# Performance work log

Measured on AMD Instinct MI355X. Metric: run time of the kernel, lower is better.

## Reference

```python
import jax, jax.numpy as jnp
import numpy as np

N, E = 100000, 1600000
IN, H, Z, C = 64, 128, 64, 2


def _glorot(key, fan_in, fan_out):
    s = jnp.sqrt(2.0 / (fan_in + fan_out)).astype(jnp.float32)
    return jax.random.normal(key, (fan_in, fan_out), dtype=jnp.float32) * s


def setup_inputs() -> dict:
    key = jax.random.key(0)
    ks = jax.random.split(key, 16)
    dims = [(IN, H), (H, H), (H, Z), (H, H), (H, Z), (Z, H), (H, H), (H, IN * C)]
    names = ['in', 'mu0', 'mu', 'si0', 'si', 'z', 'd0', 'out']
    inp = {
        'x': jax.random.normal(ks[0], (N, IN), dtype=jnp.float32),
        'eps': jax.random.normal(ks[1], (N, Z), dtype=jnp.float32),
        'edge_index': jax.random.randint(ks[2], (2, E), 0, N, dtype=jnp.int64),
    }
    for i, (nm, (fi, fo)) in enumerate(zip(names, dims)):
        inp[f'w_{nm}'] = _glorot(ks[3 + i], fi, fo)
        inp[f'b_{nm}'] = jnp.zeros((fo,), dtype=jnp.float32)
    return inp


def _gcn(x, W, b, src, dst, dinv):
    # PyG GCNConv: symmetric normalization with self-loops.
    h = x @ W                                      # [N, d_out]
    norm = (dinv[src] * dinv[dst])[:, None]        # [E, 1]
    agg = jax.ops.segment_sum(h[src] * norm, dst, num_segments=N)
    agg = agg + h * (dinv * dinv)[:, None]         # self-loop term (norm = 1/deg)
    return agg + b


def reference(x, edge_index, eps,
              w_in, b_in, w_mu0, b_mu0, w_mu, b_mu,
              w_si0, b_si0, w_si, b_si,
              w_z, b_z, w_d0, b_d0, w_out, b_out):
    src, dst = edge_index[0], edge_index[1]
    deg = jax.ops.segment_sum(jnp.ones((E,), jnp.float32), dst, num_segments=N) + 1.0
    dinv = jax.lax.rsqrt(deg)
    # encode
    h = jax.nn.relu(_gcn(x, w_in, b_in, src, dst, dinv))
    mu = jax.nn.relu(_gcn(h, w_mu0, b_mu0, src, dst, dinv))
    mu = jax.nn.relu(_gcn(mu, w_mu, b_mu, src, dst, dinv))
    si = jax.nn.relu(_gcn(h, w_si0, b_si0, src, dst, dinv))
    si = jax.nn.sigmoid(_gcn(si, w_si, b_si, src, dst, dinv))
    # reparameterize
    z = mu + si * eps
    # decode (first decoder layer has no activation, per the original forward)
    r = _gcn(z, w_z, b_z, src, dst, dinv)
    r = jax.nn.relu(_gcn(r, w_d0, b_d0, src, dst, dinv))
    logits = _gcn(r, w_out, b_out, src, dst, dinv)   # [N, IN*C]
    logits = logits.reshape(-1, C)                   # [N*IN, C]
    return logits, mu, si
```

## Files before the change

### kernel.cpp

```cpp
#include <hip/hip_runtime.h>


typedef short bf16x8 __attribute__((ext_vector_type(8)));
typedef float f32x4 __attribute__((ext_vector_type(4)));

__device__ __forceinline__ ushort f2bf(float f) {
    uint x = __float_as_uint(f);
    uint r = x + 0x7FFFu + ((x >> 16) & 1u);
    return (ushort)(r >> 16);
}
__device__ __forceinline__ float bf2f(ushort h) {
    return __uint_as_float(((uint)h) << 16);
}

__global__ void count_deg_kernel(const int* __restrict__ dst, int* __restrict__ deg, int E) {
    int i = blockIdx.x * blockDim.x + threadIdx.x;
    if (i < E) atomicAdd(&deg[dst[i]], 1);
}

__global__ void dinv_kernel(const int* __restrict__ deg, float* __restrict__ dinv, int N) {
    int i = blockIdx.x * blockDim.x + threadIdx.x;
    if (i < N) dinv[i] = rsqrtf((float)(deg[i] + 1));
}

__global__ __launch_bounds__(1024) void scan_block_kernel(const int* __restrict__ deg,
                                                          int* __restrict__ row_start,
                                                          int* __restrict__ bsum, int n) {
    __shared__ int s[1024];
    int i = blockIdx.x * 1024 + threadIdx.x;
    int v = (i < n) ? deg[i] : 0;
    s[threadIdx.x] = v;
    __syncthreads();
    for (int off = 1; off < 1024; off <<= 1) {
        int t = (threadIdx.x >= off) ? s[threadIdx.x - off] : 0;
        __syncthreads();
        s[threadIdx.x] += t;
        __syncthreads();
    }
    if (i < n) row_start[i] = s[threadIdx.x] - v;
    if (threadIdx.x == 1023) bsum[blockIdx.x] = s[1023];
}

__global__ __launch_bounds__(1024) void scan_partials_kernel(int* __restrict__ bsum, int nb) {
    __shared__ int s[1024];
    int v = (threadIdx.x < nb) ? bsum[threadIdx.x] : 0;
    s[threadIdx.x] = v;
    __syncthreads();
    for (int off = 1; off < 1024; off <<= 1) {
        int t = (threadIdx.x >= off) ? s[threadIdx.x - off] : 0;
        __syncthreads();
        s[threadIdx.x] += t;
        __syncthreads();
    }
    if (threadIdx.x < nb) bsum[threadIdx.x] = s[threadIdx.x] - v;
}

__global__ __launch_bounds__(1024) void scan_add_kernel(int* __restrict__ row_start,
                                                        const int* __restrict__ bsum, int N, int E) {
    int i = blockIdx.x * 1024 + threadIdx.x;
    if (i < N) row_start[i] += bsum[blockIdx.x];
    if (i == 0) row_start[N] = E;
}

__global__ void place_kernel(const int* __restrict__ src, const int* __restrict__ dst,
                             const int* __restrict__ row_start, int* __restrict__ cnt,
                             int2* __restrict__ csr, const float* __restrict__ dinv, int E) {
    int i = blockIdx.x * blockDim.x + threadIdx.x;
    if (i < E) {
        int d = dst[i], s = src[i];
        int pos = row_start[d] + atomicAdd(&cnt[d], 1);
        csr[pos] = make_int2(s, __float_as_int(dinv[s] * dinv[d]));
    }
}

__global__ void rowsum_kernel(const int2* __restrict__ csr, const int* __restrict__ row_start,
                              const float* __restrict__ dinv, float* __restrict__ cvec, int N) {
    int j = blockIdx.x * blockDim.x + threadIdx.x;
    if (j >= N) return;
    float s = dinv[j] * dinv[j];
    int b = row_start[j], e = row_start[j + 1];
    for (int k = b; k < e; ++k) s += __int_as_float(csr[k].y);
    cvec[j] = s;
}

__global__ void wc_kernel(const float* __restrict__ w_z, const float* __restrict__ b_z,
                          const float* __restrict__ w_d0,
                          float* __restrict__ Wc, float* __restrict__ bzw) {
    int o = blockIdx.x * 256 + threadIdx.x;
    if (o >= 65 * 128) return;
    int i = o >> 7, j = o & 127;
    float s = 0.f;
    for (int k = 0; k < 128; ++k) {
        float a = (i < 64) ? w_z[i * 128 + k] : b_z[k];
        s = fmaf(a, w_d0[k * 128 + j], s);
    }
    if (i < 64) Wc[i * 128 + j] = s;
    else        bzw[j] = s;
}

__global__ void pack_kernel(const float* __restrict__ W, ushort* __restrict__ Wp, int KI, int KO) {
    int idx = blockIdx.x * 256 + threadIdx.x;
    if (idx >= KI * KO) return;
    int e = idx & 7, l = (idx >> 3) & 63, t = idx >> 9;
    int KB = KI / 32;
    int c = t / KB, kb = t % KB;
    int k = kb * 32 + (l >> 4) * 8 + e, col = c * 16 + (l & 15);
    Wp[idx] = f2bf(W[(size_t)k * KO + col]);
}

__global__ void cvt8_kernel(const float* __restrict__ in, ushort* __restrict__ out, int n8) {
    int i = blockIdx.x * 256 + threadIdx.x;
    if (i >= n8) return;
    float4 a = ((const float4*)in)[i * 2];
    float4 b = ((const float4*)in)[i * 2 + 1];
    bf16x8 o;
    o[0] = (short)f2bf(a.x); o[1] = (short)f2bf(a.y);
    o[2] = (short)f2bf(a.z); o[3] = (short)f2bf(a.w);
    o[4] = (short)f2bf(b.x); o[5] = (short)f2bf(b.y);
    o[6] = (short)f2bf(b.z); o[7] = (short)f2bf(b.w);
    ((bf16x8*)out)[i] = o;
}

template <int W, int EPI, int OUT>
__global__ __launch_bounds__(256) void bprop_kernel(const ushort* __restrict__ xb, void* __restrict__ outp,
                                                    const int* __restrict__ row_start,
                                                    const int2* __restrict__ csr,
                                                    const float* __restrict__ dinv,
                                                    const float* __restrict__ bias,
                                                    const float* __restrict__ mu,
                                                    const float* __restrict__ eps,
                                                    ushort* __restrict__ zout, int N) {
    constexpr int L = W / 8;
    constexpr int EPL = 64 / L;
    int wave = threadIdx.x >> 6, lane = threadIdx.x & 63;
    int node = blockIdx.x * 4 + wave;
    if (node >= N) return;
    int sub = lane / L, f8 = lane % L;
    int beg = row_start[node], end = row_start[node + 1];
    float d2 = dinv[node]; d2 = d2 * d2;

    float a0[8] = {}, a1[8] = {};
    for (int base = beg; base < end; base += 2 * EPL) {
        int e0 = base + sub, e1 = base + EPL + sub;
        int2 p0 = csr[e0 < end ? e0 : 0];
        int2 p1 = csr[e1 < end ? e1 : 0];
        float w0 = (e0 < end) ? __int_as_float(p0.y) : 0.f;
        float w1 = (e1 < end) ? __int_as_float(p1.y) : 0.f;
        bf16x8 v0 = *(const bf16x8*)(xb + (size_t)p0.x * W + f8 * 8);
        bf16x8 v1 = *(const bf16x8*)(xb + (size_t)p1.x * W + f8 * 8);
        #pragma unroll
        for (int i = 0; i < 8; ++i) a0[i] = fmaf(w0, bf2f((ushort)v0[i]), a0[i]);
        #pragma unroll
        for (int i = 0; i < 8; ++i) a1[i] = fmaf(w1, bf2f((ushort)v1[i]), a1[i]);
    }
    float acc[8];
    #pragma unroll
    for (int i = 0; i < 8; ++i) acc[i] = a0[i] + a1[i];
    #pragma unroll
    for (int m = L; m < 64; m <<= 1) {
        #pragma unroll
        for (int i = 0; i < 8; ++i) acc[i] += __shfl_xor(acc[i], m);
    }
    if (sub != 0) return;

    bf16x8 sv = *(const bf16x8*)(xb + (size_t)node * W + f8 * 8);
    #pragma unroll
    for (int i = 0; i < 8; ++i) acc[i] = fmaf(d2, bf2f((ushort)sv[i]), acc[i]);

    if constexpr (EPI >= 1) {
        float4 b0 = *(const float4*)&bias[f8 * 8];
        float4 b1 = *(const float4*)&bias[f8 * 8 + 4];
        float bv[8] = {b0.x, b0.y, b0.z, b0.w, b1.x, b1.y, b1.z, b1.w};
        if constexpr (EPI == 1) {
            #pragma unroll
            for (int i = 0; i < 8; ++i) acc[i] = fmaxf(acc[i] + bv[i], 0.f);
        } else {
            #pragma unroll
            for (int i = 0; i < 8; ++i) acc[i] = 1.f / (1.f + __expf(-(acc[i] + bv[i])));
        }
    }

    if constexpr (OUT == 0) {
        bf16x8 o;
        #pragma unroll
        for (int i = 0; i < 8; ++i) o[i] = (short)f2bf(acc[i]);
        ((bf16x8*)outp)[(size_t)node * L + f8] = o;
    } else {
        float* of = (float*)outp;
        *(float4*)&of[(size_t)node * W + f8 * 8]     = make_float4(acc[0], acc[1], acc[2], acc[3]);
        *(float4*)&of[(size_t)node * W + f8 * 8 + 4] = make_float4(acc[4], acc[5], acc[6], acc[7]);
    }
    if constexpr (EPI == 2) {
        float4 m0 = *(const float4*)&mu[(size_t)node * W + f8 * 8];
        float4 m1 = *(const float4*)&mu[(size_t)node * W + f8 * 8 + 4];
        float4 e0 = *(const float4*)&eps[(size_t)node * W + f8 * 8];
        float4 e1 = *(const float4*)&eps[(size_t)node * W + f8 * 8 + 4];
        float mv[8] = {m0.x, m0.y, m0.z, m0.w, m1.x, m1.y, m1.z, m1.w};
        float ev[8] = {e0.x, e0.y, e0.z, e0.w, e1.x, e1.y, e1.z, e1.w};
        bf16x8 z;
        #pragma unroll
        for (int i = 0; i < 8; ++i) z[i] = (short)f2bf(fmaf(acc[i], ev[i], mv[i]));
        ((bf16x8*)zout)[(size_t)node * L + f8] = z;
    }
}

template <int KI, int KO, int EPI, int OUT>
__global__ __launch_bounds__(256) void mgemm_kernel(const ushort* __restrict__ Xb,
                                                    const bf16x8* __restrict__ Wp,
                                                    const float* __restrict__ bias,
                                                    const float* __restrict__ bias2,
                                                    const float* __restrict__ cvec,
                                                    void* __restrict__ outp, int N) {
    constexpr int KB = KI / 32;
    constexpr int CT = KO / 16;
    constexpr size_t LSB = (OUT == 1) ? (size_t)64 * KO * 4 : (size_t)64 * KO * 2;
    __shared__ __align__(16) char LsRaw[LSB];

    int w = threadIdx.x >> 6, l = threadIdx.x & 63;
    int lr = l & 15, lk = l >> 4;
    int rowbase = blockIdx.x * 64;
    int r0 = rowbase + w * 16;

    int arow = r0 + lr; if (arow > N - 1) arow = N - 1;
    bf16x8 a[KB];
    const ushort* xp = Xb + (size_t)arow * KI + lk * 8;
    #pragma unroll
    for (int kb = 0; kb < KB; ++kb) a[kb] = *(const bf16x8*)(xp + kb * 32);

    float cv[4];
    if constexpr (EPI == 3) {
        #pragma unroll
        for (int r = 0; r < 4; ++r) {
            int rr = r0 + lk * 4 + r;
            cv[r] = cvec[rr < N ? rr : 0];
        }
    }

    #pragma unroll
    for (int c = 0; c < CT; ++c) {
        f32x4 acc = {0.f, 0.f, 0.f, 0.f};
        #pragma unroll
        for (int kb = 0; kb < KB; ++kb)
            acc = __builtin_amdgcn_mfma_f32_16x16x32_bf16(a[kb], Wp[((size_t)c * KB + kb) * 64 + l], acc, 0, 0, 0);
        int col = c * 16 + lr;
        float bv = 0.f, b2v = 0.f;
        if constexpr (EPI >= 1) bv = bias[col];
        if constexpr (EPI == 3) b2v = bias2[col];
        #pragma unroll
        for (int r = 0; r < 4; ++r) {
            float v = acc[r];
            if constexpr (EPI == 1) v += bv;
            if constexpr (EPI == 2) v = fmaxf(v + bv, 0.f);
            if constexpr (EPI == 3) v = fmaxf(v + cv[r] * bv + b2v, 0.f);
            int rl = w * 16 + lk * 4 + r;
            if constexpr (OUT == 0) ((ushort*)LsRaw)[(size_t)rl * KO + col] = f2bf(v);
            else                    ((float*)LsRaw)[(size_t)rl * KO + col] = v;
        }
    }
    __syncthreads();

    if constexpr (OUT == 0) {
        ushort* o = (ushort*)outp;
        constexpr int CH = 64 * KO / 8;
        for (int idx = threadIdx.x; idx < CH; idx += 256) {
            int row = idx / (KO / 8), c8 = idx % (KO / 8);
            if (rowbase + row < N)
                *(bf16x8*)(o + (size_t)(rowbase + row) * KO + c8 * 8) = ((const bf16x8*)LsRaw)[idx];
        }
    } else {
        float* o = (float*)outp;
        constexpr int CH = 64 * KO / 4;
        for (int idx = threadIdx.x; idx < CH; idx += 256) {
            int row = idx / (KO / 4), c4 = idx % (KO / 4);
            if (rowbase + row < N)
                *(float4*)(o + (size_t)(rowbase + row) * KO + c4 * 4) = ((const float4*)LsRaw)[idx];
        }
    }
}

extern "C" void kernel_launch(void* const* d_in, const int* in_sizes, int n_in,
                              void* d_out, int out_size, void* d_ws, size_t ws_size,
                              hipStream_t stream) {
    const float* x    = (const float*)d_in[0];
    const float* eps  = (const float*)d_in[1];
    const int*   ei   = (const int*)d_in[2];
    const float* w_in  = (const float*)d_in[3];  const float* b_in  = (const float*)d_in[4];
    const float* w_mu0 = (const float*)d_in[5];  const float* b_mu0 = (const float*)d_in[6];
    const float* w_mu  = (const float*)d_in[7];  const float* b_mu  = (const float*)d_in[8];
    const float* w_si0 = (const float*)d_in[9];  const float* b_si0 = (const float*)d_in[10];
    const float* w_si  = (const float*)d_in[11]; const float* b_si  = (const float*)d_in[12];
    const float* w_z   = (const float*)d_in[13]; const float* b_z   = (const float*)d_in[14];
    const float* w_d0  = (const float*)d_in[15]; const float* b_d0  = (const float*)d_in[16];
    const float* w_out = (const float*)d_in[17]; const float* b_out = (const float*)d_in[18];

    const int N = in_sizes[0] / 64;
    const int E = in_sizes[2] / 2;
    const int* srcI = ei;
    const int* dstI = ei + E;

    auto align = [](size_t v) { return (v + 255) & ~(size_t)255; };
    char* w = (char*)d_ws;
    size_t off = 0;
    int*    deg       = (int*)(w + off);    off = align(off + (size_t)N * 4);
    float*  cvec      = (float*)(w + off);  off = align(off + (size_t)N * 4);
    int*    row_start = (int*)(w + off);    off = align(off + (size_t)(N + 1) * 4);
    int*    bsum      = (int*)(w + off);    off = align(off + 1024 * 4);
    float*  dinv      = (float*)(w + off);  off = align(off + (size_t)N * 4);
    float*  Wc        = (float*)(w + off);  off = align(off + 64 * 128 * 4);
    float*  bzw       = (float*)(w + off);  off = align(off + 128 * 4);
    ushort* P_in      = (ushort*)(w + off); off = align(off + 64 * 128 * 2);
    ushort* P_mu0     = (ushort*)(w + off); off = align(off + 128 * 128 * 2);
    ushort* P_si0     = (ushort*)(w + off); off = align(off + 128 * 128 * 2);
    ushort* P_mu      = (ushort*)(w + off); off = align(off + 128 * 64 * 2);
    ushort* P_si      = (ushort*)(w + off); off = align(off + 128 * 64 * 2);
    ushort* P_wc      = (ushort*)(w + off); off = align(off + 64 * 128 * 2);
    ushort* P_out     = (ushort*)(w + off); off = align(off + 128 * 128 * 2);
    int2*   csr       = (int2*)(w + off);   off = align(off + (size_t)E * 8);
    ushort* xb        = (ushort*)(w + off); off = align(off + (size_t)N * 64 * 2);
    ushort* Ab        = (ushort*)(w + off); off = align(off + (size_t)N * 128 * 2);
    ushort* Ab0 = Ab;
    ushort* Ab1 = Ab + (size_t)N * 64;

    float* Cc = (float*)d_out;
    float* M  = Cc + (size_t)N * 128;
    float* S  = M + (size_t)N * 64;
    ushort* Cb_x = (ushort*)Cc;
    ushort* Cb_y = (ushort*)(Cc + (size_t)N * 64);
    ushort* Db_x = (ushort*)M;

    const int TB = 256;
    hipMemsetAsync(deg, 0, (size_t)N * 4, stream);
    count_deg_kernel<<<(E + TB - 1) / TB, TB, 0, stream>>>(dstI, deg, E);
    dinv_kernel<<<(N + TB - 1) / TB, TB, 0, stream>>>(deg, dinv, N);
    int nb = (N + 1023) / 1024;
    scan_block_kernel<<<nb, 1024, 0, stream>>>(deg, row_start, bsum, N);
    scan_partials_kernel<<<1, 1024, 0, stream>>>(bsum, nb);
    scan_add_kernel<<<nb, 1024, 0, stream>>>(row_start, bsum, N, E);
    hipMemsetAsync(deg, 0, (size_t)N * 4, stream);
    place_kernel<<<(E + TB - 1) / TB, TB, 0, stream>>>(srcI, dstI, row_start, deg, csr, dinv, E);
    rowsum_kernel<<<(N + TB - 1) / TB, TB, 0, stream>>>(csr, row_start, dinv, cvec, N);
    wc_kernel<<<(65 * 128 + 255) / 256, 256, 0, stream>>>(w_z, b_z, w_d0, Wc, bzw);

    pack_kernel<<<(64 * 128 + 255) / 256, 256, 0, stream>>>(w_in, P_in, 64, 128);
    pack_kernel<<<(128 * 128 + 255) / 256, 256, 0, stream>>>(w_mu0, P_mu0, 128, 128);
    pack_kernel<<<(128 * 128 + 255) / 256, 256, 0, stream>>>(w_si0, P_si0, 128, 128);
    pack_kernel<<<(128 * 64 + 255) / 256, 256, 0, stream>>>(w_mu, P_mu, 128, 64);
    pack_kernel<<<(128 * 64 + 255) / 256, 256, 0, stream>>>(w_si, P_si, 128, 64);
    pack_kernel<<<(64 * 128 + 255) / 256, 256, 0, stream>>>(Wc, P_wc, 64, 128);
    pack_kernel<<<(128 * 128 + 255) / 256, 256, 0, stream>>>(w_out, P_out, 128, 128);
    cvt8_kernel<<<((N * 8) + 255) / 256, 256, 0, stream>>>(x, xb, N * 8);

    int pgrid = (N + 3) / 4;
    int ggrid = (N + 63) / 64;

    bprop_kernel<64, 0, 0><<<pgrid, 256, 0, stream>>>(xb, Ab0, row_start, csr, dinv, nullptr, nullptr, nullptr, nullptr, N);
    mgemm_kernel<64, 128, 2, 0><<<ggrid, 256, 0, stream>>>(Ab0, (const bf16x8*)P_in, b_in, nullptr, nullptr, Cb_x, N);
    bprop_kernel<128, 0, 0><<<pgrid, 256, 0, stream>>>(Cb_x, Db_x, row_start, csr, dinv, nullptr, nullptr, nullptr, nullptr, N);
    mgemm_kernel<128, 128, 2, 0><<<ggrid, 256, 0, stream>>>(Db_x, (const bf16x8*)P_mu0, b_mu0, nullptr, nullptr, Ab, N);
    mgemm_kernel<128, 128, 2, 0><<<ggrid, 256, 0, stream>>>(Db_x, (const bf16x8*)P_si0, b_si0, nullptr, nullptr, Cb_x, N);
    mgemm_kernel<128, 64, 0, 0><<<ggrid, 256, 0, stream>>>(Ab, (const bf16x8*)P_mu, nullptr, nullptr, nullptr, Cb_y, N);
    bprop_kernel<64, 1, 1><<<pgrid, 256, 0, stream>>>(Cb_y, M, row_start, csr, dinv, b_mu, nullptr, nullptr, nullptr, N);
    mgemm_kernel<128, 64, 0, 0><<<ggrid, 256, 0, stream>>>(Cb_x, (const bf16x8*)P_si, nullptr, nullptr, nullptr, Ab0, N);
    bprop_kernel<64, 2, 1><<<pgrid, 256, 0, stream>>>(Ab0, S, row_start, csr, dinv, b_si, M, eps, Ab1, N);
    bprop_kernel<64, 0, 0><<<pgrid, 256, 0, stream>>>(Ab1, Cb_y, row_start, csr, dinv, nullptr, nullptr, nullptr, nullptr, N);
    bprop_kernel<64, 0, 0><<<pgrid, 256, 0, stream>>>(Cb_y, Ab0, row_start, csr, dinv, nullptr, nullptr, nullptr, nullptr, N);
    mgemm_kernel<64, 128, 3, 0><<<ggrid, 256, 0, stream>>>(Ab0, (const bf16x8*)P_wc, bzw, b_d0, cvec, Cb_x, N);
    bprop_kernel<128, 0, 0><<<pgrid, 256, 0, stream>>>(Cb_x, Ab, row_start, csr, dinv, nullptr, nullptr, nullptr, nullptr, N);
    mgemm_kernel<128, 128, 1, 1><<<ggrid, 256, 0, stream>>>(Ab, (const bf16x8*)P_out, b_out, nullptr, nullptr, Cc, N);
}
```

Baseline: 622.1 us.

## Fuse gather with MFMA GEMMs per layer and bin edges before CSR placement

Aggregation (gather over CSR) and the following bf16 MFMA GEMMs are fused into single kernels per layer that stage 64-row tiles in LDS. The mu and sigma encoder branches now share one gathered tile, and their two 64-wide outputs are packed into one 128-wide buffer so they are propagated together. This removes intermediate global round-trips and many launches. CSR construction gains a two-pass binned scatter meant to improve locality of the placement atomics, and the weight pack kernels are merged into one launch. The cost is that gather work runs serialized before the GEMM within a block, with lower occupancy from larger LDS use, and there are extra passes over the edges.

New measurement: 809.1 us. 1.3x slower.

```diff
diff --git a/kernel.cpp b/kernel.cpp
--- a/kernel.cpp
+++ b/kernel.cpp
@@ -13,9 +13,22 @@
     return __uint_as_float(((uint)h) << 16);
 }
 
-__global__ void count_deg_kernel(const int* __restrict__ dst, int* __restrict__ deg, int E) {
-    int i = blockIdx.x * blockDim.x + threadIdx.x;
-    if (i < E) atomicAdd(&deg[dst[i]], 1);
+__global__ __launch_bounds__(1024) void counts_kernel(const int* __restrict__ dst,
+        int* __restrict__ deg, int* __restrict__ bc0, int E, int NB, int shift) {
+    __shared__ int h[8192];
+    for (int j = threadIdx.x; j < NB; j += 1024) h[j] = 0;
+    __syncthreads();
+    int stride = gridDim.x * 1024;
+    for (int i = blockIdx.x * 1024 + threadIdx.x; i < E; i += stride) {
+        int d = dst[i];
+        atomicAdd(&deg[d], 1);
+        atomicAdd(&h[d >> shift], 1);
+    }
+    __syncthreads();
+    for (int j = threadIdx.x; j < NB; j += 1024) {
+        int v = h[j];
+        if (v) atomicAdd(&bc0[j], v);
+    }
 }
 
 __global__ void dinv_kernel(const int* __restrict__ deg, float* __restrict__ dinv, int N) {
@@ -23,12 +36,12 @@
     if (i < N) dinv[i] = rsqrtf((float)(deg[i] + 1));
 }
 
-__global__ __launch_bounds__(1024) void scan_block_kernel(const int* __restrict__ deg,
-                                                          int* __restrict__ row_start,
+__global__ __launch_bounds__(1024) void scan_block_kernel(const int* __restrict__ in,
+                                                          int* __restrict__ out,
                                                           int* __restrict__ bsum, int n) {
     __shared__ int s[1024];
     int i = blockIdx.x * 1024 + threadIdx.x;
-    int v = (i < n) ? deg[i] : 0;
+    int v = (i < n) ? in[i] : 0;
     s[threadIdx.x] = v;
     __syncthreads();
     for (int off = 1; off < 1024; off <<= 1) {
@@ -37,7 +50,7 @@
         s[threadIdx.x] += t;
         __syncthreads();
     }
-    if (i < n) row_start[i] = s[threadIdx.x] - v;
+    if (i < n) out[i] = s[threadIdx.x] - v;
     if (threadIdx.x == 1023) bsum[blockIdx.x] = s[1023];
 }
 
@@ -55,21 +68,33 @@
     if (threadIdx.x < nb) bsum[threadIdx.x] = s[threadIdx.x] - v;
 }
 
-__global__ __launch_bounds__(1024) void scan_add_kernel(int* __restrict__ row_start,
-                                                        const int* __restrict__ bsum, int N, int E) {
+__global__ __launch_bounds__(1024) void scan_add_kernel(int* __restrict__ arr,
+                                                        const int* __restrict__ bsum, int n, int total) {
     int i = blockIdx.x * 1024 + threadIdx.x;
-    if (i < N) row_start[i] += bsum[blockIdx.x];
-    if (i == 0) row_start[N] = E;
-}
-
-__global__ void place_kernel(const int* __restrict__ src, const int* __restrict__ dst,
-                             const int* __restrict__ row_start, int* __restrict__ cnt,
-                             int2* __restrict__ csr, const float* __restrict__ dinv, int E) {
+    if (i < n) arr[i] += bsum[blockIdx.x];
+    if (i == 0) arr[n] = total;
+}
+
+__global__ void scatter_kernel(const int* __restrict__ src, const int* __restrict__ dst,
+                               const int* __restrict__ bin_start, int* __restrict__ bc1,
+                               int2* __restrict__ ebuf, int E, int shift) {
     int i = blockIdx.x * blockDim.x + threadIdx.x;
     if (i < E) {
-        int d = dst[i], s = src[i];
-        int pos = row_start[d] + atomicAdd(&cnt[d], 1);
-        csr[pos] = make_int2(s, __float_as_int(dinv[s] * dinv[d]));
+        int d = dst[i];
+        int b = d >> shift;
+        int pos = bin_start[b] + atomicAdd(&bc1[b], 1);
+        ebuf[pos] = make_int2(src[i], d);
+    }
+}
+
+__global__ void place2_kernel(const int2* __restrict__ ebuf, const int* __restrict__ row_start,
+                              int* __restrict__ cnt, int2* __restrict__ csr,
+                              const float* __restrict__ dinv, int E) {
+    int i = blockIdx.x * blockDim.x + threadIdx.x;
+    if (i < E) {
+        int2 e = ebuf[i];
+        int pos = row_start[e.y] + atomicAdd(&cnt[e.y], 1);
+        csr[pos] = make_int2(e.x, __float_as_int(dinv[e.x] * dinv[e.y]));
     }
 }
 
@@ -83,9 +108,9 @@
     cvec[j] = s;
 }
 
-__global__ void wc_kernel(const float* __restrict__ w_z, const float* __restrict__ b_z,
-                          const float* __restrict__ w_d0,
-                          float* __restrict__ Wc, float* __restrict__ bzw) {
+__global__ void wcpack_kernel(const float* __restrict__ w_z, const float* __restrict__ b_z,
+                              const float* __restrict__ w_d0,
+                              ushort* __restrict__ P_wc, float* __restrict__ bzw) {
     int o = blockIdx.x * 256 + threadIdx.x;
     if (o >= 65 * 128) return;
     int i = o >> 7, j = o & 127;
@@ -94,18 +119,33 @@
         float a = (i < 64) ? w_z[i * 128 + k] : b_z[k];
         s = fmaf(a, w_d0[k * 128 + j], s);
     }
-    if (i < 64) Wc[i * 128 + j] = s;
-    else        bzw[j] = s;
-}
-
-__global__ void pack_kernel(const float* __restrict__ W, ushort* __restrict__ Wp, int KI, int KO) {
-    int idx = blockIdx.x * 256 + threadIdx.x;
+    if (i < 64) {
+        int c = j >> 4, kb = i >> 5, l = ((i >> 3) & 3) * 16 + (j & 15), e = i & 7;
+        P_wc[(size_t)((c * 2 + kb) * 64 + l) * 8 + e] = f2bf(s);
+    } else bzw[j] = s;
+}
+
+__device__ __forceinline__ void pack_one(const float* __restrict__ W, ushort* __restrict__ P,
+                                         int KI, int KO, int idx) {
     if (idx >= KI * KO) return;
     int e = idx & 7, l = (idx >> 3) & 63, t = idx >> 9;
     int KB = KI / 32;
     int c = t / KB, kb = t % KB;
-    int k = kb * 32 + (l >> 4) * 8 + e, col = c * 16 + (l & 15);
-    Wp[idx] = f2bf(W[(size_t)k * KO + col]);
+    int k = kb * 32 + ((l >> 4) << 3) + e, col = c * 16 + (l & 15);
+    P[idx] = f2bf(W[(size_t)k * KO + col]);
+}
+
+__global__ void megapack_kernel(const float* w_in, const float* w_mu0, const float* w_si0,
+                                const float* w_mu, const float* w_si, const float* w_out,
+                                ushort* P_in, ushort* P_mu0, ushort* P_si0,
+                                ushort* P_mu, ushort* P_si, ushort* P_out) {
+    int b = blockIdx.x, tid = threadIdx.x;
+    if (b < 32)       pack_one(w_in,  P_in,  64, 128,  (b - 0)   * 256 + tid);
+    else if (b < 96)  pack_one(w_mu0, P_mu0, 128, 128, (b - 32)  * 256 + tid);
+    else if (b < 160) pack_one(w_si0, P_si0, 128, 128, (b - 96)  * 256 + tid);
+    else if (b < 192) pack_one(w_mu,  P_mu,  128, 64,  (b - 160) * 256 + tid);
+    else if (b < 224) pack_one(w_si,  P_si,  128, 64,  (b - 192) * 256 + tid);
+    else              pack_one(w_out, P_out, 128, 128, (b - 224) * 256 + tid);
 }
 
 __global__ void cvt8_kernel(const float* __restrict__ in, ushort* __restrict__ out, int n8) {
@@ -121,24 +161,194 @@
     ((bf16x8*)out)[i] = o;
 }
 
-template <int W, int EPI, int OUT>
-__global__ __launch_bounds__(256) void bprop_kernel(const ushort* __restrict__ xb, void* __restrict__ outp,
-                                                    const int* __restrict__ row_start,
-                                                    const int2* __restrict__ csr,
-                                                    const float* __restrict__ dinv,
-                                                    const float* __restrict__ bias,
-                                                    const float* __restrict__ mu,
-                                                    const float* __restrict__ eps,
-                                                    ushort* __restrict__ zout, int N) {
-    constexpr int L = W / 8;
-    constexpr int EPL = 64 / L;
+
+template <int WI>
+__device__ __forceinline__ void gather_phase(char* Ls, const ushort* __restrict__ xb,
+        const int* __restrict__ row_start, const int2* __restrict__ csr,
+        const float* __restrict__ dinv, int rowbase, int N, int tid) {
+    constexpr int L = WI / 8, EPL = 64 / L;
+    constexpr int STR = WI * 2 + 16;
+    int w = tid >> 6, lane = tid & 63;
+    int sub = lane / L, f8 = lane % L;
+    #pragma unroll 1
+    for (int i = 0; i < 16; ++i) {
+        int lrow = w * 16 + i;
+        int node = rowbase + lrow;
+        float acc[8] = {0.f, 0.f, 0.f, 0.f, 0.f, 0.f, 0.f, 0.f};
+        if (node < N) {
+            int beg = row_start[node], end = row_start[node + 1];
+            float d2 = dinv[node]; d2 *= d2;
+            float a0[8] = {}, a1[8] = {};
+            for (int base = beg; base < end; base += 2 * EPL) {
+                int e0 = base + sub, e1 = base + EPL + sub;
+                int2 p0 = csr[e0 < end ? e0 : 0];
+                int2 p1 = csr[e1 < end ? e1 : 0];
+                float w0 = (e0 < end) ? __int_as_float(p0.y) : 0.f;
+                float w1 = (e1 < end) ? __int_as_float(p1.y) : 0.f;
+                bf16x8 v0 = *(const bf16x8*)(xb + (size_t)p0.x * WI + f8 * 8);
+                bf16x8 v1 = *(const bf16x8*)(xb + (size_t)p1.x * WI + f8 * 8);
+                #pragma unroll
+                for (int q = 0; q < 8; ++q) a0[q] = fmaf(w0, bf2f((ushort)v0[q]), a0[q]);
+                #pragma unroll
+                for (int q = 0; q < 8; ++q) a1[q] = fmaf(w1, bf2f((ushort)v1[q]), a1[q]);
+            }
+            #pragma unroll
+            for (int q = 0; q < 8; ++q) acc[q] = a0[q] + a1[q];
+            #pragma unroll
+            for (int m = L; m < 64; m <<= 1) {
+                #pragma unroll
+                for (int q = 0; q < 8; ++q) acc[q] += __shfl_xor(acc[q], m);
+            }
+            bf16x8 sv = *(const bf16x8*)(xb + (size_t)node * WI + f8 * 8);
+            #pragma unroll
+            for (int q = 0; q < 8; ++q) acc[q] = fmaf(d2, bf2f((ushort)sv[q]), acc[q]);
+        }
+        if (sub == 0) {
+            bf16x8 o;
+            #pragma unroll
+            for (int q = 0; q < 8; ++q) o[q] = (short)f2bf(acc[q]);
+            *(bf16x8*)(Ls + lrow * STR + f8 * 16) = o;
+        }
+    }
+}
+
+template <int KI, int KO>
+__device__ __forceinline__ void mfma_phase(const char* Ls, const bf16x8* __restrict__ Wp,
+                                           float (*acc)[4], int tid) {
+    constexpr int KB = KI / 32, CT = KO / 16, STR = KI * 2 + 16;
+    int w = tid >> 6, l = tid & 63;
+    int row = w * 16 + (l & 15);
+    int lk = l >> 4;
+    bf16x8 a[KB];
+    #pragma unroll
+    for (int kb = 0; kb < KB; ++kb)
+        a[kb] = *(const bf16x8*)(Ls + row * STR + kb * 64 + lk * 16);
+    #pragma unroll
+    for (int c = 0; c < CT; ++c) {
+        f32x4 v = {0.f, 0.f, 0.f, 0.f};
+        #pragma unroll
+        for (int kb = 0; kb < KB; ++kb)
+            v = __builtin_amdgcn_mfma_f32_16x16x32_bf16(a[kb], Wp[((size_t)c * KB + kb) * 64 + l], v, 0, 0, 0);
+        acc[c][0] = v[0]; acc[c][1] = v[1]; acc[c][2] = v[2]; acc[c][3] = v[3];
+    }
+}
+
+template <int DW>
+__device__ __forceinline__ void cstore_bf16(char* Ls, const float* v, int cbase, int tid) {
+    constexpr int STR = DW * 2 + 16;
+    int w = tid >> 6, l = tid & 63;
+    int col = cbase + (l & 15);
+    int row0 = w * 16 + (l >> 4) * 4;
+    #pragma unroll
+    for (int r = 0; r < 4; ++r)
+        *(ushort*)(Ls + (row0 + r) * STR + col * 2) = f2bf(v[r]);
+}
+
+template <int KO>
+__device__ __forceinline__ void flush_bf16(const char* Ls, ushort* __restrict__ out,
+                                           int rowbase, int N, int tid) {
+    constexpr int STR = KO * 2 + 16, CH = 64 * KO / 8;
+    for (int idx = tid; idx < CH; idx += 256) {
+        int row = idx / (KO / 8), sl = idx % (KO / 8);
+        if (rowbase + row < N) {
+            bf16x8 vv = *(const bf16x8*)(Ls + row * STR + sl * 16);
+            *(bf16x8*)(out + (size_t)(rowbase + row) * KO + sl * 8) = vv;
+        }
+    }
+}
+
+__global__ __launch_bounds__(256) void fused_h_kernel(const ushort* __restrict__ xb,
+        const int* __restrict__ row_start, const int2* __restrict__ csr,
+        const float* __restrict__ dinv, const bf16x8* __restrict__ Wp,
+        const float* __restrict__ bias, ushort* __restrict__ out, int N) {
+    __shared__ __align__(16) char Ls[64 * (128 * 2 + 16)];
+    int tid = threadIdx.x;
+    int rowbase = blockIdx.x * 64;
+    gather_phase<64>(Ls, xb, row_start, csr, dinv, rowbase, N, tid);
+    __syncthreads();
+    float acc[8][4];
+    mfma_phase<64, 128>(Ls, Wp, acc, tid);
+    __syncthreads();
+    int l = tid & 63;
+    #pragma unroll
+    for (int c = 0; c < 8; ++c) {
+        float bv = bias[c * 16 + (l & 15)];
+        float v[4];
+        #pragma unroll
+        for (int r = 0; r < 4; ++r) v[r] = fmaxf(acc[c][r] + bv, 0.f);
+        cstore_bf16<128>(Ls, v, c * 16, tid);
+    }
+    __syncthreads();
+    flush_bf16<128>(Ls, out, rowbase, N, tid);
+}
+
+__global__ __launch_bounds__(256) void fused_enc_kernel(const ushort* __restrict__ hb,
+        const int* __restrict__ row_start, const int2* __restrict__ csr,
+        const float* __restrict__ dinv,
+        const bf16x8* __restrict__ P_mu0, const float* __restrict__ b_mu0,
+        const bf16x8* __restrict__ P_mu,
+        const bf16x8* __restrict__ P_si0, const float* __restrict__ b_si0,
+        const bf16x8* __restrict__ P_si,
+        ushort* __restrict__ T, int N) {
+    constexpr int SEG = 64 * (128 * 2 + 16);
+    __shared__ __align__(16) char Ls[2 * SEG];
+    char* L0 = Ls;
+    char* L1 = Ls + SEG;
+    int tid = threadIdx.x;
+    int rowbase = blockIdx.x * 64;
+    int l = tid & 63;
+
+    gather_phase<128>(L0, hb, row_start, csr, dinv, rowbase, N, tid);
+    __syncthreads();
+
+    float acc[8][4];
+    mfma_phase<128, 128>(L0, P_mu0, acc, tid);
+    #pragma unroll
+    for (int c = 0; c < 8; ++c) {
+        float bv = b_mu0[c * 16 + (l & 15)];
+        float v[4];
+        #pragma unroll
+        for (int r = 0; r < 4; ++r) v[r] = fmaxf(acc[c][r] + bv, 0.f);
+        cstore_bf16<128>(L1, v, c * 16, tid);
+    }
+    __syncthreads();
+    float rmu[4][4];
+    mfma_phase<128, 64>(L1, P_mu, rmu, tid);
+    __syncthreads();
+    mfma_phase<128, 128>(L0, P_si0, acc, tid);
+    #pragma unroll
+    for (int c = 0; c < 8; ++c) {
+        float bv = b_si0[c * 16 + (l & 15)];
+        float v[4];
+        #pragma unroll
+        for (int r = 0; r < 4; ++r) v[r] = fmaxf(acc[c][r] + bv, 0.f);
+        cstore_bf16<128>(L1, v, c * 16, tid);
+    }
+    __syncthreads();
+    float rsi[4][4];
+    mfma_phase<128, 64>(L1, P_si, rsi, tid);
+    __syncthreads();
+    #pragma unroll
+    for (int c = 0; c < 4; ++c) {
+        cstore_bf16<128>(L0, rmu[c], c * 16, tid);
+        cstore_bf16<128>(L0, rsi[c], 64 + c * 16, tid);
+    }
+    __syncthreads();
+    flush_bf16<128>(L0, T, rowbase, N, tid);
+}
+
+__global__ __launch_bounds__(256) void mssz_kernel(const ushort* __restrict__ T,
+        const int* __restrict__ row_start, const int2* __restrict__ csr,
+        const float* __restrict__ dinv, const float* __restrict__ b_mu,
+        const float* __restrict__ b_si, const float* __restrict__ eps,
+        float* __restrict__ M, float* __restrict__ S, ushort* __restrict__ zb, int N) {
+    constexpr int L = 16, EPL = 4;
     int wave = threadIdx.x >> 6, lane = threadIdx.x & 63;
     int node = blockIdx.x * 4 + wave;
     if (node >= N) return;
     int sub = lane / L, f8 = lane % L;
     int beg = row_start[node], end = row_start[node + 1];
-    float d2 = dinv[node]; d2 = d2 * d2;
-
+    float d2 = dinv[node]; d2 *= d2;
     float a0[8] = {}, a1[8] = {};
     for (int base = beg; base < end; base += 2 * EPL) {
         int e0 = base + sub, e1 = base + EPL + sub;
@@ -146,134 +356,161 @@
         int2 p1 = csr[e1 < end ? e1 : 0];
         float w0 = (e0 < end) ? __int_as_float(p0.y) : 0.f;
         float w1 = (e1 < end) ? __int_as_float(p1.y) : 0.f;
-        bf16x8 v0 = *(const bf16x8*)(xb + (size_t)p0.x * W + f8 * 8);
-        bf16x8 v1 = *(const bf16x8*)(xb + (size_t)p1.x * W + f8 * 8);
-        #pragma unroll
-        for (int i = 0; i < 8; ++i) a0[i] = fmaf(w0, bf2f((ushort)v0[i]), a0[i]);
-        #pragma unroll
-        for (int i = 0; i < 8; ++i) a1[i] = fmaf(w1, bf2f((ushort)v1[i]), a1[i]);
+        bf16x8 v0 = *(const bf16x8*)(T + (size_t)p0.x * 128 + f8 * 8);
+        bf16x8 v1 = *(const bf16x8*)(T + (size_t)p1.x * 128 + f8 * 8);
+        #pragma unroll
+        for (int q = 0; q < 8; ++q) a0[q] = fmaf(w0, bf2f((ushort)v0[q]), a0[q]);
+        #pragma unroll
+        for (int q = 0; q < 8; ++q) a1[q] = fmaf(w1, bf2f((ushort)v1[q]), a1[q]);
     }
     float acc[8];
     #pragma unroll
-    for (int i = 0; i < 8; ++i) acc[i] = a0[i] + a1[i];
-    #pragma unroll
-    for (int m = L; m < 64; m <<= 1) {
-        #pragma unroll
-        for (int i = 0; i < 8; ++i) acc[i] += __shfl_xor(acc[i], m);
+    for (int q = 0; q < 8; ++q) acc[q] = a0[q] + a1[q];
+    #pragma unroll
+    for (int m = 16; m < 64; m <<= 1) {
+        #pragma unroll
+        for (int q = 0; q < 8; ++q) acc[q] += __shfl_xor(acc[q], m);
     }
     if (sub != 0) return;
-
-    bf16x8 sv = *(const bf16x8*)(xb + (size_t)node * W + f8 * 8);
-    #pragma unroll
-    for (int i = 0; i < 8; ++i) acc[i] = fmaf(d2, bf2f((ushort)sv[i]), acc[i]);
-
-    if constexpr (EPI >= 1) {
-        float4 b0 = *(const float4*)&bias[f8 * 8];
-        float4 b1 = *(const float4*)&bias[f8 * 8 + 4];
-        float bv[8] = {b0.x, b0.y, b0.z, b0.w, b1.x, b1.y, b1.z, b1.w};
-        if constexpr (EPI == 1) {
-            #pragma unroll
-            for (int i = 0; i < 8; ++i) acc[i] = fmaxf(acc[i] + bv[i], 0.f);
-        } else {
-            #pragma unroll
-            for (int i = 0; i < 8; ++i) acc[i] = 1.f / (1.f + __expf(-(acc[i] + bv[i])));
-        }
-    }
-
-    if constexpr (OUT == 0) {
-        bf16x8 o;
-        #pragma unroll
-        for (int i = 0; i < 8; ++i) o[i] = (short)f2bf(acc[i]);
-        ((bf16x8*)outp)[(size_t)node * L + f8] = o;
+    bf16x8 sv = *(const bf16x8*)(T + (size_t)node * 128 + f8 * 8);
+    #pragma unroll
+    for (int q = 0; q < 8; ++q) acc[q] = fmaf(d2, bf2f((ushort)sv[q]), acc[q]);
+
+    bool is_mu = (f8 < 8);
+    const float* bp = is_mu ? b_mu : b_si;
+    int o = (f8 & 7) * 8;
+    float val[8];
+    #pragma unroll
+    for (int q = 0; q < 8; ++q) {
+        float t = acc[q] + bp[o + q];
+        val[q] = is_mu ? fmaxf(t, 0.f) : 1.f / (1.f + __expf(-t));
+    }
+    if (is_mu) {
+        *(float4*)&M[(size_t)node * 64 + o]     = make_float4(val[0], val[1], val[2], val[3]);
+        *(float4*)&M[(size_t)node * 64 + o + 4] = make_float4(val[4], val[5], val[6], val[7]);
     } else {
-        float* of = (float*)outp;
-        *(float4*)&of[(size_t)node * W + f8 * 8]     = make_float4(acc[0], acc[1], acc[2], acc[3]);
-        *(float4*)&of[(size_t)node * W + f8 * 8 + 4] = make_float4(acc[4], acc[5], acc[6], acc[7]);
-    }
-    if constexpr (EPI == 2) {
-        float4 m0 = *(const float4*)&mu[(size_t)node * W + f8 * 8];
-        float4 m1 = *(const float4*)&mu[(size_t)node * W + f8 * 8 + 4];
-        float4 e0 = *(const float4*)&eps[(size_t)node * W + f8 * 8];
-        float4 e1 = *(const float4*)&eps[(size_t)node * W + f8 * 8 + 4];
-        float mv[8] = {m0.x, m0.y, m0.z, m0.w, m1.x, m1.y, m1.z, m1.w};
-        float ev[8] = {e0.x, e0.y, e0.z, e0.w, e1.x, e1.y, e1.z, e1.w};
+        *(float4*)&S[(size_t)node * 64 + o]     = make_float4(val[0], val[1], val[2], val[3]);
+        *(float4*)&S[(size_t)node * 64 + o + 4] = make_float4(val[4], val[5], val[6], val[7]);
+    }
+    float oth[8];
+    #pragma unroll
+    for (int q = 0; q < 8; ++q) oth[q] = __shfl_xor(val[q], 8);
+    if (is_mu) {
+        float4 e0v = *(const float4*)&eps[(size_t)node * 64 + o];
+        float4 e1v = *(const float4*)&eps[(size_t)node * 64 + o + 4];
+        float ev[8] = {e0v.x, e0v.y, e0v.z, e0v.w, e1v.x, e1v.y, e1v.z, e1v.w};
         bf16x8 z;
         #pragma unroll
-        for (int i = 0; i < 8; ++i) z[i] = (short)f2bf(fmaf(acc[i], ev[i], mv[i]));
-        ((bf16x8*)zout)[(size_t)node * L + f8] = z;
-    }
-}
-
-template <int KI, int KO, int EPI, int OUT>
-__global__ __launch_bounds__(256) void mgemm_kernel(const ushort* __restrict__ Xb,
-                                                    const bf16x8* __restrict__ Wp,
-                                                    const float* __restrict__ bias,
-                                                    const float* __restrict__ bias2,
-                                                    const float* __restrict__ cvec,
-                                                    void* __restrict__ outp, int N) {
-    constexpr int KB = KI / 32;
-    constexpr int CT = KO / 16;
-    constexpr size_t LSB = (OUT == 1) ? (size_t)64 * KO * 4 : (size_t)64 * KO * 2;
-    __shared__ __align__(16) char LsRaw[LSB];
-
-    int w = threadIdx.x >> 6, l = threadIdx.x & 63;
-    int lr = l & 15, lk = l >> 4;
+        for (int q = 0; q < 8; ++q) z[q] = (short)f2bf(fmaf(oth[q], ev[q], val[q]));
+        *(bf16x8*)(zb + (size_t)node * 64 + o) = z;
+    }
+}
+
+__global__ __launch_bounds__(256) void prop64_kernel(const ushort* __restrict__ xb,
+        ushort* __restrict__ out, const int* __restrict__ row_start,
+        const int2* __restrict__ csr, const float* __restrict__ dinv, int N) {
+    constexpr int L = 8, EPL = 8;
+    int wave = threadIdx.x >> 6, lane = threadIdx.x & 63;
+    int node = blockIdx.x * 4 + wave;
+    if (node >= N) return;
+    int sub = lane / L, f8 = lane % L;
+    int beg = row_start[node], end = row_start[node + 1];
+    float d2 = dinv[node]; d2 *= d2;
+    float a0[8] = {}, a1[8] = {};
+    for (int base = beg; base < end; base += 2 * EPL) {
+        int e0 = base + sub, e1 = base + EPL + sub;
+        int2 p0 = csr[e0 < end ? e0 : 0];
+        int2 p1 = csr[e1 < end ? e1 : 0];
+        float w0 = (e0 < end) ? __int_as_float(p0.y) : 0.f;
+        float w1 = (e1 < end) ? __int_as_float(p1.y) : 0.f;
+        bf16x8 v0 = *(const bf16x8*)(xb + (size_t)p0.x * 64 + f8 * 8);
+        bf16x8 v1 = *(const bf16x8*)(xb + (size_t)p1.x * 64 + f8 * 8);
+        #pragma unroll
+        for (int q = 0; q < 8; ++q) a0[q] = fmaf(w0, bf2f((ushort)v0[q]), a0[q]);
+        #pragma unroll
+        for (int q = 0; q < 8; ++q) a1[q] = fmaf(w1, bf2f((ushort)v1[q]), a1[q]);
+    }
+    float acc[8];
+    #pragma unroll
+    for (int q = 0; q < 8; ++q) acc[q] = a0[q] + a1[q];
+    #pragma unroll
+    for (int m = 8; m < 64; m <<= 1) {
+        #pragma unroll
+        for (int q = 0; q < 8; ++q) acc[q] += __shfl_xor(acc[q], m);
+    }
+    if (sub != 0) return;
+    bf16x8 sv = *(const bf16x8*)(xb + (size_t)node * 64 + f8 * 8);
+    bf16x8 oz;
+    #pragma unroll
+    for (int q = 0; q < 8; ++q) oz[q] = (short)f2bf(fmaf(d2, bf2f((ushort)sv[q]), acc[q]));
+    *(bf16x8*)(out + (size_t)node * 64 + f8 * 8) = oz;
+}
+
+__global__ __launch_bounds__(256) void fused_r2_kernel(const ushort* __restrict__ pzb,
+        const int* __restrict__ row_start, const int2* __restrict__ csr,
+        const float* __restrict__ dinv, const bf16x8* __restrict__ Wp,
+        const float* __restrict__ bzw, const float* __restrict__ b_d0,
+        const float* __restrict__ cvec, ushort* __restrict__ out, int N) {
+    __shared__ __align__(16) char Ls[64 * (128 * 2 + 16)];
+    int tid = threadIdx.x;
     int rowbase = blockIdx.x * 64;
-    int r0 = rowbase + w * 16;
-
-    int arow = r0 + lr; if (arow > N - 1) arow = N - 1;
-    bf16x8 a[KB];
-    const ushort* xp = Xb + (size_t)arow * KI + lk * 8;
-    #pragma unroll
-    for (int kb = 0; kb < KB; ++kb) a[kb] = *(const bf16x8*)(xp + kb * 32);
-
-    float cv[4];
-    if constexpr (EPI == 3) {
-        #pragma unroll
-        for (int r = 0; r < 4; ++r) {
-            int rr = r0 + lk * 4 + r;
-            cv[r] = cvec[rr < N ? rr : 0];
-        }
-    }
-
-    #pragma unroll
-    for (int c = 0; c < CT; ++c) {
-        f32x4 acc = {0.f, 0.f, 0.f, 0.f};
-        #pragma unroll
-        for (int kb = 0; kb < KB; ++kb)
-            acc = __builtin_amdgcn_mfma_f32_16x16x32_bf16(a[kb], Wp[((size_t)c * KB + kb) * 64 + l], acc, 0, 0, 0);
-        int col = c * 16 + lr;
-        float bv = 0.f, b2v = 0.f;
-        if constexpr (EPI >= 1) bv = bias[col];
-        if constexpr (EPI == 3) b2v = bias2[col];
-        #pragma unroll
-        for (int r = 0; r < 4; ++r) {
-            float v = acc[r];
-            if constexpr (EPI == 1) v += bv;
-            if constexpr (EPI == 2) v = fmaxf(v + bv, 0.f);
-            if constexpr (EPI == 3) v = fmaxf(v + cv[r] * bv + b2v, 0.f);
-            int rl = w * 16 + lk * 4 + r;
-            if constexpr (OUT == 0) ((ushort*)LsRaw)[(size_t)rl * KO + col] = f2bf(v);
-            else                    ((float*)LsRaw)[(size_t)rl * KO + col] = v;
-        }
-    }
-    __syncthreads();
-
-    if constexpr (OUT == 0) {
-        ushort* o = (ushort*)outp;
-        constexpr int CH = 64 * KO / 8;
-        for (int idx = threadIdx.x; idx < CH; idx += 256) {
-            int row = idx / (KO / 8), c8 = idx % (KO / 8);
-            if (rowbase + row < N)
-                *(bf16x8*)(o + (size_t)(rowbase + row) * KO + c8 * 8) = ((const bf16x8*)LsRaw)[idx];
-        }
-    } else {
-        float* o = (float*)outp;
-        constexpr int CH = 64 * KO / 4;
-        for (int idx = threadIdx.x; idx < CH; idx += 256) {
-            int row = idx / (KO / 4), c4 = idx % (KO / 4);
-            if (rowbase + row < N)
-                *(float4*)(o + (size_t)(rowbase + row) * KO + c4 * 4) = ((const float4*)LsRaw)[idx];
+    gather_phase<64>(Ls, pzb, row_start, csr, dinv, rowbase, N, tid);
+    __syncthreads();
+    float acc[8][4];
+    mfma_phase<64, 128>(Ls, Wp, acc, tid);
+    __syncthreads();
+    int l = tid & 63;
+    int w = tid >> 6;
+    int row0 = rowbase + w * 16 + (l >> 4) * 4;
+    float cvr[4];
+    #pragma unroll
+    for (int r = 0; r < 4; ++r) {
+        int rr = row0 + r;
+        cvr[r] = cvec[rr < N ? rr : 0];
+    }
+    #pragma unroll
+    for (int c = 0; c < 8; ++c) {
+        int col = c * 16 + (l & 15);
+        float bz = bzw[col], bd = b_d0[col];
+        float v[4];
+        #pragma unroll
+        for (int r = 0; r < 4; ++r) v[r] = fmaxf(fmaf(cvr[r], bz, acc[c][r]) + bd, 0.f);
+        cstore_bf16<128>(Ls, v, c * 16, tid);
+    }
+    __syncthreads();
+    flush_bf16<128>(Ls, out, rowbase, N, tid);
+}
+
+__global__ __launch_bounds__(256) void fused_out_kernel(const ushort* __restrict__ r2b,
+        const int* __restrict__ row_start, const int2* __restrict__ csr,
+        const float* __restrict__ dinv, const bf16x8* __restrict__ Wp,
+        const float* __restrict__ bias, float* __restrict__ out, int N) {
+    __shared__ __align__(16) char Ls[64 * (128 * 4 + 16)];
+    int tid = threadIdx.x;
+    int rowbase = blockIdx.x * 64;
+    gather_phase<128>(Ls, r2b, row_start, csr, dinv, rowbase, N, tid);
+    __syncthreads();
+    float acc[8][4];
+    mfma_phase<128, 128>(Ls, Wp, acc, tid);
+    __syncthreads();
+    int l = tid & 63;
+    int w = tid >> 6;
+    constexpr int OSTR = 128 * 4 + 16;
+    int row0 = w * 16 + (l >> 4) * 4;
+    #pragma unroll
+    for (int c = 0; c < 8; ++c) {
+        int col = c * 16 + (l & 15);
+        float bv = bias[col];
+        #pragma unroll
+        for (int r = 0; r < 4; ++r)
+            *(float*)(Ls + (row0 + r) * OSTR + col * 4) = acc[c][r] + bv;
+    }
+    __syncthreads();
+    for (int idx = tid; idx < 64 * 32; idx += 256) {
+        int row = idx >> 5, sl = idx & 31;
+        if (rowbase + row < N) {
+            f32x4 v = *(const f32x4*)(Ls + row * OSTR + sl * 16);
+            *(f32x4*)(out + (size_t)(rowbase + row) * 128 + sl * 4) = v;
         }
     }
 }
@@ -298,73 +535,77 @@
     const int* srcI = ei;
     const int* dstI = ei + E;
 
+    int shift = 4;
+    while (((N >> shift) + 1) > 8192) shift++;
+    const int NB = (N >> shift) + 1;
+
     auto align = [](size_t v) { return (v + 255) & ~(size_t)255; };
-    char* w = (char*)d_ws;
+    char* wsp = (char*)d_ws;
     size_t off = 0;
-    int*    deg       = (int*)(w + off);    off = align(off + (size_t)N * 4);
-    float*  cvec      = (float*)(w + off);  off = align(off + (size_t)N * 4);
-    int*    row_start = (int*)(w + off);    off = align(off + (size_t)(N + 1) * 4);
-    int*    bsum      = (int*)(w + off);    off = align(off + 1024 * 4);
-    float*  dinv      = (float*)(w + off);  off = align(off + (size_t)N * 4);
-    float*  Wc        = (float*)(w + off);  off = align(off + 64 * 128 * 4);
-    float*  bzw       = (float*)(w + off);  off = align(off + 128 * 4);
-    ushort* P_in      = (ushort*)(w + off); off = align(off + 64 * 128 * 2);
-    ushort* P_mu0     = (ushort*)(w + off); off = align(off + 128 * 128 * 2);
-    ushort* P_si0     = (ushort*)(w + off); off = align(off + 128 * 128 * 2);
-    ushort* P_mu      = (ushort*)(w + off); off = align(off + 128 * 64 * 2);
-    ushort* P_si      = (ushort*)(w + off); off = align(off + 128 * 64 * 2);
-    ushort* P_wc      = (ushort*)(w + off); off = align(off + 64 * 128 * 2);
-    ushort* P_out     = (ushort*)(w + off); off = align(off + 128 * 128 * 2);
-    int2*   csr       = (int2*)(w + off);   off = align(off + (size_t)E * 8);
-    ushort* xb        = (ushort*)(w + off); off = align(off + (size_t)N * 64 * 2);
-    ushort* Ab        = (ushort*)(w + off); off = align(off + (size_t)N * 128 * 2);
-    ushort* Ab0 = Ab;
-    ushort* Ab1 = Ab + (size_t)N * 64;
+    int*    deg       = (int*)(wsp + off);    size_t deg_off = off; off = align(off + (size_t)N * 4);
+    int*    bc0       = (int*)(wsp + off);    off = align(off + (size_t)NB * 4);
+    int*    bc1       = (int*)(wsp + off);    off = align(off + (size_t)NB * 4);
+    size_t  zero_span = off - deg_off;
+    float*  cvec      = (float*)(wsp + off);  off = align(off + (size_t)N * 4);
+    int*    row_start = (int*)(wsp + off);    off = align(off + (size_t)(N + 1) * 4);
+    int*    bin_start = (int*)(wsp + off);    off = align(off + (size_t)(NB + 1) * 4);
+    int*    bsum      = (int*)(wsp + off);    off = align(off + 1024 * 4);
+    float*  dinv      = (float*)(wsp + off);  off = align(off + (size_t)N * 4);
+    float*  bzw       = (float*)(wsp + off);  off = align(off + 128 * 4);
+    ushort* P_in      = (ushort*)(wsp + off); off = align(off + 64 * 128 * 2);
+    ushort* P_mu0     = (ushort*)(wsp + off); off = align(off + 128 * 128 * 2);
+    ushort* P_si0     = (ushort*)(wsp + off); off = align(off + 128 * 128 * 2);
+    ushort* P_mu      = (ushort*)(wsp + off); off = align(off + 128 * 64 * 2);
+    ushort* P_si      = (ushort*)(wsp + off); off = align(off + 128 * 64 * 2);
+    ushort* P_wc      = (ushort*)(wsp + off); off = align(off + 64 * 128 * 2);
+    ushort* P_out     = (ushort*)(wsp + off); off = align(off + 128 * 128 * 2);
+    int2*   csr       = (int2*)(wsp + off);   off = align(off + (size_t)E * 8);
+    int2*   ebuf      = (int2*)(wsp + off);   off = align(off + (size_t)E * 8);
+    ushort* xb        = (ushort*)ebuf;
+    ushort* B1        = (ushort*)(wsp + off); off = align(off + (size_t)N * 128 * 2);
 
     float* Cc = (float*)d_out;
     float* M  = Cc + (size_t)N * 128;
     float* S  = M + (size_t)N * 64;
-    ushort* Cb_x = (ushort*)Cc;
-    ushort* Cb_y = (ushort*)(Cc + (size_t)N * 64);
-    ushort* Db_x = (ushort*)M;
+    ushort* T  = (ushort*)Cc;
+    ushort* zb = B1;
+    ushort* pzb = xb;
+    ushort* r2b = B1;
 
     const int TB = 256;
+    hipMemsetAsync(deg, 0, zero_span, stream);
+    counts_kernel<<<256, 1024, 0, stream>>>(dstI, deg, bc0, E, NB, shift);
+    dinv_kernel<<<(N + TB - 1) / TB, TB, 0, stream>>>(deg, dinv, N);
+    int nbN = (N + 1023) / 1024;
+    scan_block_kernel<<<nbN, 1024, 0, stream>>>(deg, row_start, bsum, N);
+    scan_partials_kernel<<<1, 1024, 0, stream>>>(bsum, nbN);
+    scan_add_kernel<<<nbN, 1024, 0, stream>>>(row_start, bsum, N, E);
+    int nbB = (NB + 1023) / 1024;
+    scan_block_kernel<<<nbB, 1024, 0, stream>>>(bc0, bin_start, bsum, NB);
+    scan_partials_kernel<<<1, 1024, 0, stream>>>(bsum, nbB);
+    scan_add_kernel<<<nbB, 1024, 0, stream>>>(bin_start, bsum, NB, E);
     hipMemsetAsync(deg, 0, (size_t)N * 4, stream);
-    count_deg_kernel<<<(E + TB - 1) / TB, TB, 0, stream>>>(dstI, deg, E);
-    dinv_kernel<<<(N + TB - 1) / TB, TB, 0, stream>>>(deg, dinv, N);
-    int nb = (N + 1023) / 1024;
-    scan_block_kernel<<<nb, 1024, 0, stream>>>(deg, row_start, bsum, N);
-    scan_partials_kernel<<<1, 1024, 0, stream>>>(bsum, nb);
-    scan_add_kernel<<<nb, 1024, 0, stream>>>(row_start, bsum, N, E);
-    hipMemsetAsync(deg, 0, (size_t)N * 4, stream);
-    place_kernel<<<(E + TB - 1) / TB, TB, 0, stream>>>(srcI, dstI, row_start, deg, csr, dinv, E);
+    scatter_kernel<<<(E + TB - 1) / TB, TB, 0, stream>>>(srcI, dstI, bin_start, bc1, ebuf, E, shift);
+    place2_kernel<<<(E + TB - 1) / TB, TB, 0, stream>>>(ebuf, row_start, deg, csr, dinv, E);
     rowsum_kernel<<<(N + TB - 1) / TB, TB, 0, stream>>>(csr, row_start, dinv, cvec, N);
-    wc_kernel<<<(65 * 128 + 255) / 256, 256, 0, stream>>>(w_z, b_z, w_d0, Wc, bzw);
-
-    pack_kernel<<<(64 * 128 + 255) / 256, 256, 0, stream>>>(w_in, P_in, 64, 128);
-    pack_kernel<<<(128 * 128 + 255) / 256, 256, 0, stream>>>(w_mu0, P_mu0, 128, 128);
-    pack_kernel<<<(128 * 128 + 255) / 256, 256, 0, stream>>>(w_si0, P_si0, 128, 128);
-    pack_kernel<<<(128 * 64 + 255) / 256, 256, 0, stream>>>(w_mu, P_mu, 128, 64);
-    pack_kernel<<<(128 * 64 + 255) / 256, 256, 0, stream>>>(w_si, P_si, 128, 64);
-    pack_kernel<<<(64 * 128 + 255) / 256, 256, 0, stream>>>(Wc, P_wc, 64, 128);
-    pack_kernel<<<(128 * 128 + 255) / 256, 256, 0, stream>>>(w_out, P_out, 128, 128);
+    wcpack_kernel<<<(65 * 128 + 255) / 256, 256, 0, stream>>>(w_z, b_z, w_d0, P_wc, bzw);
+    megapack_kernel<<<288, 256, 0, stream>>>(w_in, w_mu0, w_si0, w_mu, w_si, w_out,
+                                             P_in, P_mu0, P_si0, P_mu, P_si, P_out);
     cvt8_kernel<<<((N * 8) + 255) / 256, 256, 0, stream>>>(x, xb, N * 8);
 
-    int pgrid = (N + 3) / 4;
-    int ggrid = (N + 63) / 64;
-
-    bprop_kernel<64, 0, 0><<<pgrid, 256, 0, stream>>>(xb, Ab0, row_start, csr, dinv, nullptr, nullptr, nullptr, nullptr, N);
-    mgemm_kernel<64, 128, 2, 0><<<ggrid, 256, 0, stream>>>(Ab0, (const bf16x8*)P_in, b_in, nullptr, nullptr, Cb_x, N);
-    bprop_kernel<128, 0, 0><<<pgrid, 256, 0, stream>>>(Cb_x, Db_x, row_start, csr, dinv, nullptr, nullptr, nullptr, nullptr, N);
-    mgemm_kernel<128, 128, 2, 0><<<ggrid, 256, 0, stream>>>(Db_x, (const bf16x8*)P_mu0, b_mu0, nullptr, nullptr, Ab, N);
-    mgemm_kernel<128, 128, 2, 0><<<ggrid, 256, 0, stream>>>(Db_x, (const bf16x8*)P_si0, b_si0, nullptr, nullptr, Cb_x, N);
-    mgemm_kernel<128, 64, 0, 0><<<ggrid, 256, 0, stream>>>(Ab, (const bf16x8*)P_mu, nullptr, nullptr, nullptr, Cb_y, N);
-    bprop_kernel<64, 1, 1><<<pgrid, 256, 0, stream>>>(Cb_y, M, row_start, csr, dinv, b_mu, nullptr, nullptr, nullptr, N);
-    mgemm_kernel<128, 64, 0, 0><<<ggrid, 256, 0, stream>>>(Cb_x, (const bf16x8*)P_si, nullptr, nullptr, nullptr, Ab0, N);
-    bprop_kernel<64, 2, 1><<<pgrid, 256, 0, stream>>>(Ab0, S, row_start, csr, dinv, b_si, M, eps, Ab1, N);
-    bprop_kernel<64, 0, 0><<<pgrid, 256, 0, stream>>>(Ab1, Cb_y, row_start, csr, dinv, nullptr, nullptr, nullptr, nullptr, N);
-    bprop_kernel<64, 0, 0><<<pgrid, 256, 0, stream>>>(Cb_y, Ab0, row_start, csr, dinv, nullptr, nullptr, nullptr, nullptr, N);
-    mgemm_kernel<64, 128, 3, 0><<<ggrid, 256, 0, stream>>>(Ab0, (const bf16x8*)P_wc, bzw, b_d0, cvec, Cb_x, N);
-    bprop_kernel<128, 0, 0><<<pgrid, 256, 0, stream>>>(Cb_x, Ab, row_start, csr, dinv, nullptr, nullptr, nullptr, nullptr, N);
-    mgemm_kernel<128, 128, 1, 1><<<ggrid, 256, 0, stream>>>(Ab, (const bf16x8*)P_out, b_out, nullptr, nullptr, Cc, N);
-}
+    int GB = (N + 63) / 64;
+    int PG = (N + 3) / 4;
+
+    fused_h_kernel<<<GB, 256, 0, stream>>>(xb, row_start, csr, dinv,
+                                           (const bf16x8*)P_in, b_in, B1, N);
+    fused_enc_kernel<<<GB, 256, 0, stream>>>(B1, row_start, csr, dinv,
+                                             (const bf16x8*)P_mu0, b_mu0, (const bf16x8*)P_mu,
+                                             (const bf16x8*)P_si0, b_si0, (const bf16x8*)P_si,
+                                             T, N);
+    mssz_kernel<<<PG, 256, 0, stream>>>(T, row_start, csr, dinv, b_mu, b_si, eps, M, S, zb, N);
+    prop64_kernel<<<PG, 256, 0, stream>>>(zb, pzb, row_start, csr, dinv, N);
+    fused_r2_kernel<<<GB, 256, 0, stream>>>(pzb, row_start, csr, dinv,
+                                            (const bf16x8*)P_wc, bzw, b_d0, cvec, r2b, N);
+    fused_out_kernel<<<GB, 256, 0, stream>>>(r2b, row_start, csr, dinv,
+                                             (const bf16x8*)P_out, b_out, Cc, N);
+}
```
